# Performance work log

Hardware: AMD Instinct MI355X
Metric: run time of the kernel (lower is better)

The kernel has to match this reference:

```python
import jax, jax.numpy as jnp
import numpy as np
from jax import lax

C_IN, C_KEY, C_VAL = 1024, 256, 512

def conv3x3(x, w, b):
    # x: [B,C_in,H,W], w: [C_out,C_in,3,3] -> SAME padding, stride 1
    y = lax.conv_general_dilated(x, w, window_strides=(1, 1), padding='SAME',
                                 dimension_numbers=('NCHW', 'OIHW', 'NCHW'))
    return y + b[None, :, None, None]

def setup_inputs() -> dict:
    key = jax.random.key(0)
    ks = jax.random.split(key, 10)
    B, H, W = 16, 32, 32
    conv_std = 0.01  # matches torch init.normal_(std=0.01)
    inp = {
        'src_temp': jax.random.normal(ks[0], (B, C_IN, H, W), jnp.float32),
        'src_search': jax.random.normal(ks[1], (B, C_IN, H, W), jnp.float32),
        'wk_m': jax.random.normal(ks[2], (C_KEY, C_IN, 3, 3), jnp.float32) * conv_std,
        'bk_m': jnp.zeros((C_KEY,), jnp.float32),
        'wv_m': jax.random.normal(ks[3], (C_VAL, C_IN, 3, 3), jnp.float32) * conv_std,
        'bv_m': jnp.zeros((C_VAL,), jnp.float32),
        'wk_q': jax.random.normal(ks[4], (C_KEY, C_IN, 3, 3), jnp.float32) * conv_std,
        'bk_q': jnp.zeros((C_KEY,), jnp.float32),
        'wv_q': jax.random.normal(ks[5], (C_VAL, C_IN, 3, 3), jnp.float32) * conv_std,
        'bv_q': jnp.zeros((C_VAL,), jnp.float32),
    }
    return inp

def reference(src_temp, src_search, wk_m, bk_m, wv_m, bv_m, wk_q, bk_q, wv_q, bv_q):
    # key/value projections
    m_key = conv3x3(src_temp, wk_m, bk_m)      # [B, Ck, H, W]
    m_value = conv3x3(src_temp, wv_m, bv_m)    # [B, Cv, H, W]
    q_key = conv3x3(src_search, wk_q, bk_q)    # [B, Ck, H, W]
    q_value = conv3x3(src_search, wv_q, bv_q)  # [B, Cv, H, W]

    B, Ck, H, W = m_key.shape
    Cv = m_value.shape[1]
    HW = H * W

    mk = m_key.reshape(B, Ck, HW)   # [B, Ck, HW_m]
    qk = q_key.reshape(B, Ck, HW)   # [B, Ck, HW_q]
    # scores: [B, HW_m, HW_q]
    w = jnp.einsum('bcm,bcq->bmq', mk, qk) / jnp.sqrt(jnp.float32(Ck))
    w = jax.nn.softmax(w, axis=1)   # normalize over memory locations

    mv = m_value.reshape(B, Cv, HW)            # [B, Cv, HW_m]
    mem_info = jnp.einsum('bcm,bmq->bcq', mv, w).reshape(B, Cv, H, W)
    return jnp.concatenate([mem_info, q_value], axis=1)  # [B, 2*Cv, H, W]
```

## Files before the change

### kernel.cpp

```cpp
#include <hip/hip_runtime.h>
#include <stdint.h>

typedef __bf16 bf16;
typedef __bf16 bf16x8 __attribute__((ext_vector_type(8)));
typedef float  f32x4  __attribute__((ext_vector_type(4)));

#define OFF_AHI   0ull
#define OFF_ALO   18939904ull
#define OFF_WHI   37879808ull
#define OFF_WLO   52035584ull
#define OFF_QKEYT 67108864ull
#define OFF_MKEYT 83886080ull
#define OFF_MVAL  100663296ull
#define OFF_WATTN 0ull

__device__ __forceinline__ void split(float v, bf16& h, bf16& l) {
    h = (bf16)v;
    l = (bf16)(v - (float)h);
}

__global__ __launch_bounds__(256) void k_wt(const float* __restrict__ wk,
                                            const float* __restrict__ wv,
                                            bf16* __restrict__ Wh, bf16* __restrict__ Wl) {
    size_t id = (size_t)blockIdx.x * 256 + threadIdx.x;
    int e = (int)(id & 7);
    size_t t = id >> 3;
    int mm = (int)(t % 96); t /= 96;
    int coff = (int)(t & 3); t >>= 2;
    int cch = (int)(t & 31); t >>= 5;
    int r = (int)(t % 9);
    int mt = (int)(t / 9);
    int m = mt * 96 + mm;
    int c = cch * 32 + coff * 8 + e;
    float v = (m < 256) ? wk[((size_t)m * 1024 + c) * 9 + r]
                        : wv[((size_t)(m - 256) * 1024 + c) * 9 + r];
    bf16 h, l;
    split(v, h, l);
    Wh[id] = h; Wl[id] = l;
}

__global__ __launch_bounds__(256) void k_zero(bf16* __restrict__ Ah, bf16* __restrict__ Al) {
    int id = blockIdx.x * 256 + threadIdx.x;
    int oct = id & 127;
    int t = id >> 7;
    int pos = t % 132; t /= 132;
    int bl = t & 7, hl = t >> 3;
    int yy, xx;
    if (pos < 34)       { yy = 0;  xx = pos; }
    else if (pos < 68)  { yy = 33; xx = pos - 34; }
    else if (pos < 100) { yy = pos - 68 + 1;  xx = 0; }
    else                { yy = pos - 100 + 1; xx = 33; }
    bf16* base = hl ? Al : Ah;
    size_t off = (((size_t)bl * 34 + yy) * 34 + xx) * 1024 + (size_t)oct * 8;
    *(uint4*)(base + off) = make_uint4(0u, 0u, 0u, 0u);
}

__global__ __launch_bounds__(256) void k_transpose(const float* __restrict__ src,
                                                   bf16* __restrict__ Ah, bf16* __restrict__ Al) {
    int pt = blockIdx.x, ct = blockIdx.y, bl = blockIdx.z;
    __shared__ float tile[64][68];
    int t = threadIdx.x;
    #pragma unroll
    for (int k = 0; k < 4; ++k) {
        int idx = t + 256 * k;
        int c = idx >> 4, f4 = idx & 15;
        float4 v = *(const float4*)(src + ((size_t)bl * 1024 + ct * 64 + c) * 1024 + pt * 64 + f4 * 4);
        *(float4*)&tile[c][f4 * 4] = v;
    }
    __syncthreads();
    #pragma unroll
    for (int k = 0; k < 2; ++k) {
        int s = t + 256 * k;
        int px = s >> 3, oct = s & 7;
        bf16x8 vh, vl;
        #pragma unroll
        for (int e = 0; e < 8; ++e) {
            bf16 h, l;
            split(tile[oct * 8 + e][px], h, l);
            vh[e] = h; vl[e] = l;
        }
        int pxg = pt * 64 + px;
        int yy = (pxg >> 5) + 1, xx = (pxg & 31) + 1;
        size_t off = (((size_t)bl * 34 + yy) * 34 + xx) * 1024 + ct * 64 + oct * 8;
        *(bf16x8*)(Ah + off) = vh;
        *(bf16x8*)(Al + off) = vl;
    }
}

#define XS_STRIDE 40
__global__ __launch_bounds__(256) void k_conv(const bf16* __restrict__ Ah, const bf16* __restrict__ Al,
                                              const bf16* __restrict__ Wh, const bf16* __restrict__ Wl,
                                              const float* __restrict__ biask, const float* __restrict__ biasv,
                                              float* __restrict__ keyT, float* __restrict__ valout,
                                              int vstride, int voffs, int bglob) {
    int bl = blockIdx.x >> 3, rg = blockIdx.x & 7;
    int mt = blockIdx.y;
    int y0 = rg * 4;
    int b = bglob + bl;

    __shared__ bf16 Xs[2 * 6 * 34 * XS_STRIDE];

    int tid = threadIdx.x;
    int w = tid >> 6, l = tid & 63;
    int wm = (w & 1) * 48, wn = (w >> 1) * 64;
    int lm = l & 15, lq = l >> 4;
    int koff = lq * 8;

    f32x4 acc[3][4] = {};

    const size_t Abase = ((size_t)bl * 34 + y0) * 34 * 1024;
    const size_t wlane = (size_t)lq * 768 + (size_t)lm * 8;

    for (int cch = 0; cch < 32; ++cch) {
        int c0 = cch * 32;
        bf16x8 xv[7];
        int lidx[7];
        #pragma unroll
        for (int it = 0; it < 7; ++it) {
            int s = tid + 256 * it;
            if (s < 1632) {
                int hl = s >= 816;
                int r816 = s - hl * 816;
                int row = r816 / 136;
                int rr = r816 - row * 136;
                int px = rr >> 2, oct = rr & 3;
                const bf16* base = hl ? Al : Ah;
                xv[it] = *(const bf16x8*)(base + Abase + ((size_t)row * 34 + px) * 1024 + c0 + oct * 8);
                lidx[it] = ((hl * 6 + row) * 34 + px) * XS_STRIDE + oct * 8;
            } else lidx[it] = -1;
        }
        __syncthreads();
        #pragma unroll
        for (int it = 0; it < 7; ++it)
            if (lidx[it] >= 0) *(bf16x8*)&Xs[lidx[it]] = xv[it];
        __syncthreads();

        #pragma unroll
        for (int r = 0; r < 9; ++r) {
            int dy = r / 3, dx = r % 3;
            size_t wblk = (((size_t)mt * 9 + r) * 32 + cch) * 3072 + wlane;
            bf16x8 ah[3], al[3];
            #pragma unroll
            for (int i = 0; i < 3; ++i) {
                size_t o = wblk + (size_t)(wm + i * 16) * 8;
                ah[i] = *(const bf16x8*)(Wh + o);
                al[i] = *(const bf16x8*)(Wl + o);
            }
            #pragma unroll
            for (int j = 0; j < 4; ++j) {
                int n = wn + j * 16 + lm;
                int lbase = (((n >> 5) + dy) * 34 + (n & 31) + dx) * XS_STRIDE + koff;
                bf16x8 bh = *(const bf16x8*)&Xs[lbase];
                bf16x8 blo = *(const bf16x8*)&Xs[6 * 34 * XS_STRIDE + lbase];
                #pragma unroll
                for (int i = 0; i < 3; ++i) {
                    acc[i][j] = __builtin_amdgcn_mfma_f32_16x16x32_bf16(ah[i], bh,  acc[i][j], 0, 0, 0);
                    acc[i][j] = __builtin_amdgcn_mfma_f32_16x16x32_bf16(ah[i], blo, acc[i][j], 0, 0, 0);
                    acc[i][j] = __builtin_amdgcn_mfma_f32_16x16x32_bf16(al[i], bh,  acc[i][j], 0, 0, 0);
                }
            }
        }
    }

    int col = lm, rowb = lq * 4;
    #pragma unroll
    for (int i = 0; i < 3; ++i) {
        int ch4 = mt * 96 + wm + i * 16 + rowb;
        #pragma unroll
        for (int j = 0; j < 4; ++j) {
            int px = rg * 128 + wn + j * 16 + col;
            if (ch4 < 256) {
                #pragma unroll
                for (int e = 0; e < 4; ++e)
                    keyT[((size_t)b * 256 + ch4 + e) * 1024 + px] = acc[i][j][e] + biask[ch4 + e];
            } else {
                int cv = ch4 - 256;
                #pragma unroll
                for (int e = 0; e < 4; ++e)
                    valout[((size_t)b * vstride + voffs + cv + e) * 1024 + px] = acc[i][j][e] + biasv[cv + e];
            }
        }
    }
}

__global__ __launch_bounds__(256) void k_scores(const float* __restrict__ mkeyT,
                                                const float* __restrict__ qkeyT,
                                                float* __restrict__ wattn) {
    int mt = blockIdx.x, qt = blockIdx.y, b = blockIdx.z;
    __shared__ float As[8][64];
    __shared__ float Bs[8][64];
    int t = threadIdx.x, tx = t & 15, ty = t >> 4;
    const float* mk = mkeyT + (size_t)b * 256 * 1024 + mt * 64;
    const float* qk = qkeyT + (size_t)b * 256 * 1024 + qt * 64;
    float acc[4][4];
    #pragma unroll
    for (int i = 0; i < 4; ++i)
        #pragma unroll
        for (int j = 0; j < 4; ++j) acc[i][j] = 0.0f;

    int half = t >> 7, idx = t & 127;
    const float* stsrc = half ? qk : mk;
    for (int cc = 0; cc < 32; ++cc) {
        float4 v = *(const float4*)(stsrc + (size_t)(cc * 8 + (idx >> 4)) * 1024 + (idx & 15) * 4);
        __syncthreads();
        ((float4*)(half ? &Bs[0][0] : &As[0][0]))[idx] = v;
        __syncthreads();
        #pragma unroll
        for (int k = 0; k < 8; ++k) {
            float a[4], bb[4];
            #pragma unroll
            for (int i = 0; i < 4; ++i) a[i] = As[k][tx + 16 * i];
            #pragma unroll
            for (int j = 0; j < 4; ++j) bb[j] = Bs[k][ty + 16 * j];
            #pragma unroll
            for (int i = 0; i < 4; ++i)
                #pragma unroll
                for (int j = 0; j < 4; ++j) acc[i][j] += a[i] * bb[j];
        }
    }
    #pragma unroll
    for (int j = 0; j < 4; ++j) {
        int q = qt * 64 + ty + 16 * j;
        #pragma unroll
        for (int i = 0; i < 4; ++i) {
            int m = mt * 64 + tx + 16 * i;
            wattn[((size_t)b * 1024 + q) * 1024 + m] = acc[i][j] * 0.0625f;
        }
    }
}

__global__ __launch_bounds__(256) void k_softmax(float* __restrict__ wattn) {
    int row = blockIdx.x * 4 + (threadIdx.x >> 6);
    int l = threadIdx.x & 63;
    float* base = wattn + (size_t)row * 1024;
    float4 v[4];
    #pragma unroll
    for (int k = 0; k < 4; ++k) v[k] = *(float4*)(base + l * 4 + k * 256);
    float f[16];
    #pragma unroll
    for (int k = 0; k < 4; ++k) { f[4*k]=v[k].x; f[4*k+1]=v[k].y; f[4*k+2]=v[k].z; f[4*k+3]=v[k].w; }
    float mx = -3.0e38f;
    #pragma unroll
    for (int e = 0; e < 16; ++e) mx = fmaxf(mx, f[e]);
    #pragma unroll
    for (int off = 32; off > 0; off >>= 1) mx = fmaxf(mx, __shfl_xor(mx, off));
    float s = 0.0f;
    #pragma unroll
    for (int e = 0; e < 16; ++e) { f[e] = __expf(f[e] - mx); s += f[e]; }
    #pragma unroll
    for (int off = 32; off > 0; off >>= 1) s += __shfl_xor(s, off);
    float inv = 1.0f / s;
    #pragma unroll
    for (int k = 0; k < 4; ++k) {
        v[k].x = f[4*k] * inv; v[k].y = f[4*k+1] * inv;
        v[k].z = f[4*k+2] * inv; v[k].w = f[4*k+3] * inv;
        *(float4*)(base + l * 4 + k * 256) = v[k];
    }
}

__global__ __launch_bounds__(256) void k_memv(const float* __restrict__ mval,
                                              const float* __restrict__ wattn,
                                              float* __restrict__ outp) {
    int qt = blockIdx.x, ct = blockIdx.y, b = blockIdx.z;
    __shared__ float Aw[64][17];
    __shared__ float Bv[64][17];
    int t = threadIdx.x, tx = t & 15, ty = t >> 4;
    const float* wv_ = wattn + ((size_t)b * 1024 + qt * 64) * 1024;
    const float* mv_ = mval + ((size_t)b * 512 + ct * 64) * 1024;
    float acc[4][4];
    #pragma unroll
    for (int i = 0; i < 4; ++i)
        #pragma unroll
        for (int j = 0; j < 4; ++j) acc[i][j] = 0.0f;

    int row = t >> 2, c4 = (t & 3) * 4;
    for (int mm = 0; mm < 64; ++mm) {
        float4 va = *(const float4*)(wv_ + (size_t)row * 1024 + mm * 16 + c4);
        float4 vb = *(const float4*)(mv_ + (size_t)row * 1024 + mm * 16 + c4);
        __syncthreads();
        Aw[row][c4] = va.x; Aw[row][c4+1] = va.y; Aw[row][c4+2] = va.z; Aw[row][c4+3] = va.w;
        Bv[row][c4] = vb.x; Bv[row][c4+1] = vb.y; Bv[row][c4+2] = vb.z; Bv[row][c4+3] = vb.w;
        __syncthreads();
        #pragma unroll
        for (int k = 0; k < 16; ++k) {
            float a[4], bb[4];
            #pragma unroll
            for (int j = 0; j < 4; ++j) a[j] = Aw[tx + 16 * j][k];
            #pragma unroll
            for (int i = 0; i < 4; ++i) bb[i] = Bv[ty + 16 * i][k];
            #pragma unroll
            for (int i = 0; i < 4; ++i)
                #pragma unroll
                for (int j = 0; j < 4; ++j) acc[i][j] += bb[i] * a[j];
        }
    }
    #pragma unroll
    for (int i = 0; i < 4; ++i) {
        int cg = ct * 64 + ty + 16 * i;
        #pragma unroll
        for (int j = 0; j < 4; ++j) {
            int q = qt * 64 + tx + 16 * j;
            outp[((size_t)b * 1024 + cg) * 1024 + q] = acc[i][j];
        }
    }
}

extern "C" void kernel_launch(void* const* d_in, const int* in_sizes, int n_in,
                              void* d_out, int out_size, void* d_ws, size_t ws_size,
                              hipStream_t stream) {
    const float* src_temp   = (const float*)d_in[0];
    const float* src_search = (const float*)d_in[1];
    const float* wk_m = (const float*)d_in[2];
    const float* bk_m = (const float*)d_in[3];
    const float* wv_m = (const float*)d_in[4];
    const float* bv_m = (const float*)d_in[5];
    const float* wk_q = (const float*)d_in[6];
    const float* bk_q = (const float*)d_in[7];
    const float* wv_q = (const float*)d_in[8];
    const float* bv_q = (const float*)d_in[9];
    float* out = (float*)d_out;
    char* ws = (char*)d_ws;
    bf16* Ah = (bf16*)(ws + OFF_AHI);
    bf16* Al = (bf16*)(ws + OFF_ALO);
    bf16* Wh = (bf16*)(ws + OFF_WHI);
    bf16* Wl = (bf16*)(ws + OFF_WLO);
    float* qkeyT = (float*)(ws + OFF_QKEYT);
    float* mkeyT = (float*)(ws + OFF_MKEYT);
    float* mval  = (float*)(ws + OFF_MVAL);
    float* wattn = (float*)(ws + OFF_WATTN);

    hipLaunchKernelGGL(k_zero, dim3(1056), dim3(256), 0, stream, Ah, Al);

    hipLaunchKernelGGL(k_wt, dim3(27648), dim3(256), 0, stream, wk_q, wv_q, Wh, Wl);
    for (int h = 0; h < 2; ++h) {
        hipLaunchKernelGGL(k_transpose, dim3(16, 16, 8), dim3(256), 0, stream,
                           src_search + (size_t)h * 8 * 1024 * 1024, Ah, Al);
        hipLaunchKernelGGL(k_conv, dim3(64, 8), dim3(256), 0, stream,
                           Ah, Al, Wh, Wl, bk_q, bv_q, qkeyT, out, 1024, 512, h * 8);
    }
    hipLaunchKernelGGL(k_wt, dim3(27648), dim3(256), 0, stream, wk_m, wv_m, Wh, Wl);
    for (int h = 0; h < 2; ++h) {
        hipLaunchKernelGGL(k_transpose, dim3(16, 16, 8), dim3(256), 0, stream,
                           src_temp + (size_t)h * 8 * 1024 * 1024, Ah, Al);
        hipLaunchKernelGGL(k_conv, dim3(64, 8), dim3(256), 0, stream,
                           Ah, Al, Wh, Wl, bk_m, bv_m, mkeyT, mval, 512, 0, h * 8);
    }

    hipLaunchKernelGGL(k_scores,  dim3(16, 16, 16), dim3(256), 0, stream, mkeyT, qkeyT, wattn);
    hipLaunchKernelGGL(k_softmax, dim3(4096),       dim3(256), 0, stream, wattn);
    hipLaunchKernelGGL(k_memv,    dim3(16, 8, 16),  dim3(256), 0, stream, mval, wattn, out);
}
```

Baseline: 1.904 ms.

## Move attention score and value GEMMs to split-bf16 MFMA with packed operands

The scalar FP32 score and memory-value GEMMs are replaced with MFMA kernels that emulate fp32 through three bf16 products (hi*hi, hi*lo, lo*hi) on 128x128 tiles with register prefetch of the next K chunk. The conv epilogue and softmax now write keys, memory values and attention weights as packed hi/lo bf16 pairs in the layouts these GEMMs need, so the split is done once per element. This targets the high cost of the FP32 FMA-bound attention GEMMs, at the price of a small precision loss from dropping the lo*lo term and extra packing work in the producer kernels.

```diff
diff --git a/kernel.cpp b/kernel.cpp
--- a/kernel.cpp
+++ b/kernel.cpp
@@ -4,6 +4,7 @@
 typedef __bf16 bf16;
 typedef __bf16 bf16x8 __attribute__((ext_vector_type(8)));
 typedef float  f32x4  __attribute__((ext_vector_type(4)));
+typedef unsigned int u32;
 
 #define OFF_AHI   0ull
 #define OFF_ALO   18939904ull
@@ -17,6 +18,21 @@
 __device__ __forceinline__ void split(float v, bf16& h, bf16& l) {
     h = (bf16)v;
     l = (bf16)(v - (float)h);
+}
+
+__device__ __forceinline__ u32 packsplit(float v) {
+    bf16 h = (bf16)v;
+    bf16 l = (bf16)(v - (float)h);
+    unsigned short hu = __builtin_bit_cast(unsigned short, h);
+    unsigned short lu = __builtin_bit_cast(unsigned short, l);
+    return (u32)hu | ((u32)lu << 16);
+}
+
+__device__ __forceinline__ void deint4(const uint4 v, uint2& h, uint2& l) {
+    h.x = (v.x & 0xffffu) | (v.y << 16);
+    h.y = (v.z & 0xffffu) | (v.w << 16);
+    l.x = (v.x >> 16) | (v.y & 0xffff0000u);
+    l.y = (v.z >> 16) | (v.w & 0xffff0000u);
 }
 
 __global__ __launch_bounds__(256) void k_wt(const float* __restrict__ wk,
@@ -91,8 +107,8 @@
 __global__ __launch_bounds__(256) void k_conv(const bf16* __restrict__ Ah, const bf16* __restrict__ Al,
                                               const bf16* __restrict__ Wh, const bf16* __restrict__ Wl,
                                               const float* __restrict__ biask, const float* __restrict__ biasv,
-                                              float* __restrict__ keyT, float* __restrict__ valout,
-                                              int vstride, int voffs, int bglob) {
+                                              u32* __restrict__ keyT, float* __restrict__ valf,
+                                              u32* __restrict__ valp, int bglob) {
     int bl = blockIdx.x >> 3, rg = blockIdx.x & 7;
     int mt = blockIdx.y;
     int y0 = rg * 4;
@@ -170,61 +186,92 @@
         for (int j = 0; j < 4; ++j) {
             int px = rg * 128 + wn + j * 16 + col;
             if (ch4 < 256) {
-                #pragma unroll
-                for (int e = 0; e < 4; ++e)
-                    keyT[((size_t)b * 256 + ch4 + e) * 1024 + px] = acc[i][j][e] + biask[ch4 + e];
+                u32 p0 = packsplit(acc[i][j][0] + biask[ch4 + 0]);
+                u32 p1 = packsplit(acc[i][j][1] + biask[ch4 + 1]);
+                u32 p2 = packsplit(acc[i][j][2] + biask[ch4 + 2]);
+                u32 p3 = packsplit(acc[i][j][3] + biask[ch4 + 3]);
+                *(uint4*)(keyT + ((size_t)b * 1024 + px) * 256 + ch4) = make_uint4(p0, p1, p2, p3);
             } else {
                 int cv = ch4 - 256;
-                #pragma unroll
-                for (int e = 0; e < 4; ++e)
-                    valout[((size_t)b * vstride + voffs + cv + e) * 1024 + px] = acc[i][j][e] + biasv[cv + e];
-            }
-        }
-    }
-}
-
-__global__ __launch_bounds__(256) void k_scores(const float* __restrict__ mkeyT,
-                                                const float* __restrict__ qkeyT,
+                if (valp) {
+                    #pragma unroll
+                    for (int e = 0; e < 4; ++e)
+                        valp[((size_t)b * 512 + cv + e) * 1024 + px] = packsplit(acc[i][j][e] + biasv[cv + e]);
+                } else {
+                    #pragma unroll
+                    for (int e = 0; e < 4; ++e)
+                        valf[((size_t)b * 1024 + 512 + cv + e) * 1024 + px] = acc[i][j][e] + biasv[cv + e];
+                }
+            }
+        }
+    }
+}
+
+#define AS 40
+__global__ __launch_bounds__(256) void k_scores(const u32* __restrict__ qkT,
+                                                const u32* __restrict__ mkT,
                                                 float* __restrict__ wattn) {
     int mt = blockIdx.x, qt = blockIdx.y, b = blockIdx.z;
-    __shared__ float As[8][64];
-    __shared__ float Bs[8][64];
-    int t = threadIdx.x, tx = t & 15, ty = t >> 4;
-    const float* mk = mkeyT + (size_t)b * 256 * 1024 + mt * 64;
-    const float* qk = qkeyT + (size_t)b * 256 * 1024 + qt * 64;
-    float acc[4][4];
-    #pragma unroll
-    for (int i = 0; i < 4; ++i)
-        #pragma unroll
-        for (int j = 0; j < 4; ++j) acc[i][j] = 0.0f;
-
-    int half = t >> 7, idx = t & 127;
-    const float* stsrc = half ? qk : mk;
-    for (int cc = 0; cc < 32; ++cc) {
-        float4 v = *(const float4*)(stsrc + (size_t)(cc * 8 + (idx >> 4)) * 1024 + (idx & 15) * 4);
-        __syncthreads();
-        ((float4*)(half ? &Bs[0][0] : &As[0][0]))[idx] = v;
-        __syncthreads();
-        #pragma unroll
-        for (int k = 0; k < 8; ++k) {
-            float a[4], bb[4];
-            #pragma unroll
-            for (int i = 0; i < 4; ++i) a[i] = As[k][tx + 16 * i];
-            #pragma unroll
-            for (int j = 0; j < 4; ++j) bb[j] = Bs[k][ty + 16 * j];
-            #pragma unroll
-            for (int i = 0; i < 4; ++i)
-                #pragma unroll
-                for (int j = 0; j < 4; ++j) acc[i][j] += a[i] * bb[j];
-        }
-    }
-    #pragma unroll
-    for (int j = 0; j < 4; ++j) {
-        int q = qt * 64 + ty + 16 * j;
-        #pragma unroll
-        for (int i = 0; i < 4; ++i) {
-            int m = mt * 64 + tx + 16 * i;
-            wattn[((size_t)b * 1024 + q) * 1024 + m] = acc[i][j] * 0.0625f;
+    __shared__ bf16 Qh[128][AS], Ql[128][AS], Mh[128][AS], Ml[128][AS];
+    int t = threadIdx.x;
+    int w_ = t >> 6, l = t & 63;
+    int wq = (w_ & 1) * 64, wm = (w_ >> 1) * 64;
+    int lm = l & 15, lq = l >> 4, koff = lq * 8;
+    int srow = t >> 1, sc4 = (t & 1) * 16;
+    const u32* qbase = qkT + ((size_t)b * 1024 + qt * 128 + srow) * 256 + sc4;
+    const u32* mbase = mkT + ((size_t)b * 1024 + mt * 128 + srow) * 256 + sc4;
+    f32x4 acc[4][4] = {};
+    uint4 qv[4], mv[4];
+    #pragma unroll
+    for (int k = 0; k < 4; ++k) { qv[k] = *(const uint4*)(qbase + k * 4); mv[k] = *(const uint4*)(mbase + k * 4); }
+    for (int cc = 0; cc < 8; ++cc) {
+        __syncthreads();
+        #pragma unroll
+        for (int k = 0; k < 4; ++k) {
+            uint2 h, lo;
+            deint4(qv[k], h, lo);
+            *(uint2*)&Qh[srow][sc4 + k * 4] = h;
+            *(uint2*)&Ql[srow][sc4 + k * 4] = lo;
+            deint4(mv[k], h, lo);
+            *(uint2*)&Mh[srow][sc4 + k * 4] = h;
+            *(uint2*)&Ml[srow][sc4 + k * 4] = lo;
+        }
+        __syncthreads();
+        if (cc < 7) {
+            #pragma unroll
+            for (int k = 0; k < 4; ++k) {
+                qv[k] = *(const uint4*)(qbase + (cc + 1) * 32 + k * 4);
+                mv[k] = *(const uint4*)(mbase + (cc + 1) * 32 + k * 4);
+            }
+        }
+        bf16x8 ah[4], al[4];
+        #pragma unroll
+        for (int iq = 0; iq < 4; ++iq) {
+            ah[iq] = *(const bf16x8*)&Qh[wq + iq * 16 + lm][koff];
+            al[iq] = *(const bf16x8*)&Ql[wq + iq * 16 + lm][koff];
+        }
+        #pragma unroll
+        for (int jm = 0; jm < 4; ++jm) {
+            bf16x8 bh = *(const bf16x8*)&Mh[wm + jm * 16 + lm][koff];
+            bf16x8 bl = *(const bf16x8*)&Ml[wm + jm * 16 + lm][koff];
+            #pragma unroll
+            for (int iq = 0; iq < 4; ++iq) {
+                acc[iq][jm] = __builtin_amdgcn_mfma_f32_16x16x32_bf16(ah[iq], bh, acc[iq][jm], 0, 0, 0);
+                acc[iq][jm] = __builtin_amdgcn_mfma_f32_16x16x32_bf16(ah[iq], bl, acc[iq][jm], 0, 0, 0);
+                acc[iq][jm] = __builtin_amdgcn_mfma_f32_16x16x32_bf16(al[iq], bh, acc[iq][jm], 0, 0, 0);
+            }
+        }
+    }
+    #pragma unroll
+    for (int iq = 0; iq < 4; ++iq) {
+        int q = qt * 128 + wq + iq * 16 + lq * 4;
+        #pragma unroll
+        for (int jm = 0; jm < 4; ++jm) {
+            int m = mt * 128 + wm + jm * 16 + lm;
+            float* wp = wattn + ((size_t)b * 1024 + q) * 1024 + m;
+            #pragma unroll
+            for (int e = 0; e < 4; ++e)
+                wp[(size_t)e * 1024] = acc[iq][jm][e] * 0.0625f;
         }
     }
 }
@@ -250,57 +297,78 @@
     #pragma unroll
     for (int off = 32; off > 0; off >>= 1) s += __shfl_xor(s, off);
     float inv = 1.0f / s;
+    u32* ub = (u32*)base;
     #pragma unroll
     for (int k = 0; k < 4; ++k) {
-        v[k].x = f[4*k] * inv; v[k].y = f[4*k+1] * inv;
-        v[k].z = f[4*k+2] * inv; v[k].w = f[4*k+3] * inv;
-        *(float4*)(base + l * 4 + k * 256) = v[k];
-    }
-}
-
-__global__ __launch_bounds__(256) void k_memv(const float* __restrict__ mval,
-                                              const float* __restrict__ wattn,
+        uint4 u = make_uint4(packsplit(f[4*k]   * inv), packsplit(f[4*k+1] * inv),
+                             packsplit(f[4*k+2] * inv), packsplit(f[4*k+3] * inv));
+        *(uint4*)(ub + l * 4 + k * 256) = u;
+    }
+}
+
+__global__ __launch_bounds__(256) void k_memv(const u32* __restrict__ mvalp,
+                                              const u32* __restrict__ wattnp,
                                               float* __restrict__ outp) {
-    int qt = blockIdx.x, ct = blockIdx.y, b = blockIdx.z;
-    __shared__ float Aw[64][17];
-    __shared__ float Bv[64][17];
-    int t = threadIdx.x, tx = t & 15, ty = t >> 4;
-    const float* wv_ = wattn + ((size_t)b * 1024 + qt * 64) * 1024;
-    const float* mv_ = mval + ((size_t)b * 512 + ct * 64) * 1024;
-    float acc[4][4];
-    #pragma unroll
-    for (int i = 0; i < 4; ++i)
-        #pragma unroll
-        for (int j = 0; j < 4; ++j) acc[i][j] = 0.0f;
-
-    int row = t >> 2, c4 = (t & 3) * 4;
-    for (int mm = 0; mm < 64; ++mm) {
-        float4 va = *(const float4*)(wv_ + (size_t)row * 1024 + mm * 16 + c4);
-        float4 vb = *(const float4*)(mv_ + (size_t)row * 1024 + mm * 16 + c4);
-        __syncthreads();
-        Aw[row][c4] = va.x; Aw[row][c4+1] = va.y; Aw[row][c4+2] = va.z; Aw[row][c4+3] = va.w;
-        Bv[row][c4] = vb.x; Bv[row][c4+1] = vb.y; Bv[row][c4+2] = vb.z; Bv[row][c4+3] = vb.w;
-        __syncthreads();
-        #pragma unroll
-        for (int k = 0; k < 16; ++k) {
-            float a[4], bb[4];
-            #pragma unroll
-            for (int j = 0; j < 4; ++j) a[j] = Aw[tx + 16 * j][k];
-            #pragma unroll
-            for (int i = 0; i < 4; ++i) bb[i] = Bv[ty + 16 * i][k];
-            #pragma unroll
-            for (int i = 0; i < 4; ++i)
-                #pragma unroll
-                for (int j = 0; j < 4; ++j) acc[i][j] += bb[i] * a[j];
-        }
-    }
-    #pragma unroll
-    for (int i = 0; i < 4; ++i) {
-        int cg = ct * 64 + ty + 16 * i;
-        #pragma unroll
-        for (int j = 0; j < 4; ++j) {
-            int q = qt * 64 + tx + 16 * j;
-            outp[((size_t)b * 1024 + cg) * 1024 + q] = acc[i][j];
+    int ct = blockIdx.x, qt = blockIdx.y, b = blockIdx.z;
+    __shared__ bf16 Vh[128][AS], Vl[128][AS], Wh[128][AS], Wl[128][AS];
+    int t = threadIdx.x;
+    int w_ = t >> 6, l = t & 63;
+    int wc = (w_ & 1) * 64, wq = (w_ >> 1) * 64;
+    int lm = l & 15, lq = l >> 4, koff = lq * 8;
+    int srow = t >> 1, sc4 = (t & 1) * 16;
+    const u32* vbase = mvalp  + ((size_t)b * 512  + ct * 128 + srow) * 1024 + sc4;
+    const u32* wbase = wattnp + ((size_t)b * 1024 + qt * 128 + srow) * 1024 + sc4;
+    f32x4 acc[4][4] = {};
+    uint4 vv[4], wv[4];
+    #pragma unroll
+    for (int k = 0; k < 4; ++k) { vv[k] = *(const uint4*)(vbase + k * 4); wv[k] = *(const uint4*)(wbase + k * 4); }
+    for (int mc = 0; mc < 32; ++mc) {
+        __syncthreads();
+        #pragma unroll
+        for (int k = 0; k < 4; ++k) {
+            uint2 h, lo;
+            deint4(vv[k], h, lo);
+            *(uint2*)&Vh[srow][sc4 + k * 4] = h;
+            *(uint2*)&Vl[srow][sc4 + k * 4] = lo;
+            deint4(wv[k], h, lo);
+            *(uint2*)&Wh[srow][sc4 + k * 4] = h;
+            *(uint2*)&Wl[srow][sc4 + k * 4] = lo;
+        }
+        __syncthreads();
+        if (mc < 31) {
+            #pragma unroll
+            for (int k = 0; k < 4; ++k) {
+                vv[k] = *(const uint4*)(vbase + (mc + 1) * 32 + k * 4);
+                wv[k] = *(const uint4*)(wbase + (mc + 1) * 32 + k * 4);
+            }
+        }
+        bf16x8 ah[4], al[4];
+        #pragma unroll
+        for (int ic = 0; ic < 4; ++ic) {
+            ah[ic] = *(const bf16x8*)&Vh[wc + ic * 16 + lm][koff];
+            al[ic] = *(const bf16x8*)&Vl[wc + ic * 16 + lm][koff];
+        }
+        #pragma unroll
+        for (int jq = 0; jq < 4; ++jq) {
+            bf16x8 bh = *(const bf16x8*)&Wh[wq + jq * 16 + lm][koff];
+            bf16x8 bl = *(const bf16x8*)&Wl[wq + jq * 16 + lm][koff];
+            #pragma unroll
+            for (int ic = 0; ic < 4; ++ic) {
+                acc[ic][jq] = __builtin_amdgcn_mfma_f32_16x16x32_bf16(ah[ic], bh, acc[ic][jq], 0, 0, 0);
+                acc[ic][jq] = __builtin_amdgcn_mfma_f32_16x16x32_bf16(ah[ic], bl, acc[ic][jq], 0, 0, 0);
+                acc[ic][jq] = __builtin_amdgcn_mfma_f32_16x16x32_bf16(al[ic], bh, acc[ic][jq], 0, 0, 0);
+            }
+        }
+    }
+    #pragma unroll
+    for (int ic = 0; ic < 4; ++ic) {
+        int c = ct * 128 + wc + ic * 16 + lq * 4;
+        #pragma unroll
+        for (int jq = 0; jq < 4; ++jq) {
+            int q = qt * 128 + wq + jq * 16 + lm;
+            #pragma unroll
+            for (int e = 0; e < 4; ++e)
+                outp[((size_t)b * 1024 + c + e) * 1024 + q] = acc[ic][jq][e];
         }
     }
 }
@@ -324,10 +392,11 @@
     bf16* Al = (bf16*)(ws + OFF_ALO);
     bf16* Wh = (bf16*)(ws + OFF_WHI);
     bf16* Wl = (bf16*)(ws + OFF_WLO);
-    float* qkeyT = (float*)(ws + OFF_QKEYT);
-    float* mkeyT = (float*)(ws + OFF_MKEYT);
-    float* mval  = (float*)(ws + OFF_MVAL);
+    u32* qkP = (u32*)(ws + OFF_QKEYT);
+    u32* mkP = (u32*)(ws + OFF_MKEYT);
+    u32* mvP = (u32*)(ws + OFF_MVAL);
     float* wattn = (float*)(ws + OFF_WATTN);
+    u32* wattnP = (u32*)(ws + OFF_WATTN);
 
     hipLaunchKernelGGL(k_zero, dim3(1056), dim3(256), 0, stream, Ah, Al);
 
@@ -336,17 +405,17 @@
         hipLaunchKernelGGL(k_transpose, dim3(16, 16, 8), dim3(256), 0, stream,
                            src_search + (size_t)h * 8 * 1024 * 1024, Ah, Al);
         hipLaunchKernelGGL(k_conv, dim3(64, 8), dim3(256), 0, stream,
-                           Ah, Al, Wh, Wl, bk_q, bv_q, qkeyT, out, 1024, 512, h * 8);
+                           Ah, Al, Wh, Wl, bk_q, bv_q, qkP, out, (u32*)nullptr, h * 8);
     }
     hipLaunchKernelGGL(k_wt, dim3(27648), dim3(256), 0, stream, wk_m, wv_m, Wh, Wl);
     for (int h = 0; h < 2; ++h) {
         hipLaunchKernelGGL(k_transpose, dim3(16, 16, 8), dim3(256), 0, stream,
                            src_temp + (size_t)h * 8 * 1024 * 1024, Ah, Al);
         hipLaunchKernelGGL(k_conv, dim3(64, 8), dim3(256), 0, stream,
-                           Ah, Al, Wh, Wl, bk_m, bv_m, mkeyT, mval, 512, 0, h * 8);
-    }
-
-    hipLaunchKernelGGL(k_scores,  dim3(16, 16, 16), dim3(256), 0, stream, mkeyT, qkeyT, wattn);
-    hipLaunchKernelGGL(k_softmax, dim3(4096),       dim3(256), 0, stream, wattn);
-    hipLaunchKernelGGL(k_memv,    dim3(16, 8, 16),  dim3(256), 0, stream, mval, wattn, out);
-}
+                           Ah, Al, Wh, Wl, bk_m, bv_m, mkP, (float*)nullptr, mvP, h * 8);
+    }
+
+    hipLaunchKernelGGL(k_scores,  dim3(8, 8, 16), dim3(256), 0, stream, qkP, mkP, wattn);
+    hipLaunchKernelGGL(k_softmax, dim3(4096),     dim3(256), 0, stream, wattn);
+    hipLaunchKernelGGL(k_memv,    dim3(4, 8, 16), dim3(256), 0, stream, mvP, wattnP, out);
+}
```

Measured after the change: 1.591 ms. -16.4%, faster.
